# Optimization experiments

Hardware: AMD Instinct MI355X
Metric: run time of the kernel (lower is better)

The kernel has to match this reference:

```python
import jax, jax.numpy as jnp
import numpy as np

NEG = jnp.float32(-1e9)
N_PRE = 12000   # n_train_pre_nms (module default training=True)
N_POST = 2000   # n_train_post_nms
MIN_SIZE = 16.0
NMS_THRESH = 0.7


def _make_anchors(feat_size=64, stride=16):
    scales = np.array([128.0, 256.0, 512.0])
    ratios = np.array([0.5, 1.0, 2.0])
    ws = (scales[:, None] * np.sqrt(1.0 / ratios)[None, :]).reshape(-1)  # [9]
    hs = (scales[:, None] * np.sqrt(ratios)[None, :]).reshape(-1)        # [9]
    ctr = (np.arange(feat_size) + 0.5) * stride
    cy, cx = np.meshgrid(ctr, ctr, indexing='ij')
    cx = cx.reshape(-1, 1); cy = cy.reshape(-1, 1)                       # [4096,1]
    x1 = cx - 0.5 * ws[None, :]; y1 = cy - 0.5 * hs[None, :]
    x2 = cx + 0.5 * ws[None, :]; y2 = cy + 0.5 * hs[None, :]
    return np.stack([x1, y1, x2, y2], axis=-1).reshape(-1, 4).astype(np.float32)  # [36864,4]


def setup_inputs() -> dict:
    key = jax.random.key(0)
    k1, k2 = jax.random.split(key)
    anchors = jnp.asarray(_make_anchors())[None]            # [1, 36864, 4]
    B, N = 8, anchors.shape[1]
    pred_loc = jax.random.normal(k1, (B, N, 4), jnp.float32) * 0.2
    pred_obj = jax.random.normal(k2, (B, N, 2), jnp.float32)
    return {"img_height": 1024, "img_width": 1024,
            "anchor_boxes": anchors, "pred_loc": pred_loc, "pred_obj": pred_obj}


def _decode(anchors, loc, img_w, img_h):
    # anchors [N,4] (x1,y1,x2,y2), loc [N,4] (dx,dy,dw,dh)
    w = anchors[:, 2] - anchors[:, 0]
    h = anchors[:, 3] - anchors[:, 1]
    cx = anchors[:, 0] + 0.5 * w
    cy = anchors[:, 1] + 0.5 * h
    pcx = loc[:, 0] * w + cx
    pcy = loc[:, 1] * h + cy
    pw = jnp.exp(loc[:, 2]) * w
    ph = jnp.exp(loc[:, 3]) * h
    x1 = jnp.clip(pcx - 0.5 * pw, 0.0, img_w)
    y1 = jnp.clip(pcy - 0.5 * ph, 0.0, img_h)
    x2 = jnp.clip(pcx + 0.5 * pw, 0.0, img_w)
    y2 = jnp.clip(pcy + 0.5 * ph, 0.0, img_h)
    return jnp.stack([x1, y1, x2, y2], axis=-1)  # [N,4]


def _iou_one_vs_all(box, boxes):
    # box [4], boxes [M,4]
    ix1 = jnp.maximum(box[0], boxes[:, 0])
    iy1 = jnp.maximum(box[1], boxes[:, 1])
    ix2 = jnp.minimum(box[2], boxes[:, 2])
    iy2 = jnp.minimum(box[3], boxes[:, 3])
    inter = jnp.maximum(ix2 - ix1, 0.0) * jnp.maximum(iy2 - iy1, 0.0)
    a0 = (box[2] - box[0]) * (box[3] - box[1])
    a1 = (boxes[:, 2] - boxes[:, 0]) * (boxes[:, 3] - boxes[:, 1])
    return inter / jnp.maximum(a0 + a1 - inter, 1e-9)


def _greedy_nms(boxes, scores):
    # boxes [M,4], scores [M] (invalid entries already NEG). Selects the first
    # N_POST boxes kept by greedy IoU suppression (exactly torchvision nms +
    # [:n_post] truncation, since greedy NMS emits in descending-score order).
    def step(s, _):
        i = jnp.argmax(s)
        valid = s[i] > NEG * 0.5
        box = boxes[i]
        suppress = _iou_one_vs_all(box, boxes) > NMS_THRESH  # includes self
        s = jnp.where(suppress, NEG, s)
        return s, (box, valid)
    _, (kept, mask) = jax.lax.scan(step, scores, None, length=N_POST)
    return jnp.where(mask[:, None], kept, 0.0), mask  # [N_POST,4], [N_POST]


def reference(img_height, img_width, anchor_boxes, pred_loc, pred_obj):
    img_h = jnp.float32(img_height)
    img_w = jnp.float32(img_width)
    anchors = anchor_boxes[0]                                    # [N,4]
    scores = jax.nn.softmax(pred_obj, axis=2)[:, :, 1]           # [B,N]
    boxes = jax.vmap(lambda l: _decode(anchors, l, img_w, img_h))(pred_loc)  # [B,N,4]
    # min-size filter -> mask scores instead of dynamic filtering
    valid = jnp.all(boxes[..., 2:] - boxes[..., :2] >= MIN_SIZE, axis=-1)    # [B,N]
    scores = jnp.where(valid, scores, NEG)
    # descending sort + pre-NMS truncation == top_k
    top_s, top_i = jax.lax.top_k(scores, N_PRE)                  # [B,N_PRE]
    top_boxes = jnp.take_along_axis(boxes, top_i[..., None], axis=1)         # [B,N_PRE,4]
    kept_boxes, kept_mask = jax.vmap(_greedy_nms)(top_boxes, top_s)
    return kept_boxes, kept_mask  # [B,N_POST,4] padded, [B,N_POST] validity
```

## Files before the change

kernel.cpp:

```cpp
#include <hip/hip_runtime.h>

typedef unsigned long long u64;
typedef unsigned int u32;

#define B_SZ   8
#define N_ANC  36864
#define N_PRE  12000
#define N_POST 2000
#define SEG    2048
#define NSEG   6
#define MAXC   (SEG * NSEG)
#define NW     (SEG / 64)
#define NDW    (MAXC / 64)
#define NBLK   144

__device__ __forceinline__ float area_of(float4 p) {
  return __fmul_rn(__fsub_rn(p.z, p.x), __fsub_rn(p.w, p.y));
}

__device__ __forceinline__ bool iou_gt_a(float4 p, float4 q, float a0, float a1) {
  float ix1 = fmaxf(p.x, q.x), iy1 = fmaxf(p.y, q.y);
  float ix2 = fminf(p.z, q.z), iy2 = fminf(p.w, q.w);
  float iw = fmaxf(__fsub_rn(ix2, ix1), 0.0f);
  float ih = fmaxf(__fsub_rn(iy2, iy1), 0.0f);
  float inter = __fmul_rn(iw, ih);
  float den = fmaxf(__fsub_rn(__fadd_rn(a0, a1), inter), 1e-9f);
  return (inter / den) > 0.7f;
}

__global__ __launch_bounds__(256) void k_decode(
    const int* __restrict__ imh_p, const int* __restrict__ imw_p,
    const float* __restrict__ anchors, const float* __restrict__ loc,
    const float* __restrict__ obj, float4* __restrict__ boxes,
    u64* __restrict__ keys, u32* __restrict__ hist)
{
  __shared__ u32 lh[2048];
  int t = threadIdx.x;
#pragma unroll
  for (int i = 0; i < 8; ++i) lh[t + i * 256] = 0;
  __syncthreads();

  int n = blockIdx.x * 256 + t;
  int b = blockIdx.y;
  float a0 = anchors[n * 4 + 0], a1 = anchors[n * 4 + 1];
  float a2 = anchors[n * 4 + 2], a3 = anchors[n * 4 + 3];
  size_t off = (size_t)b * N_ANC + n;
  float l0 = loc[off * 4 + 0], l1 = loc[off * 4 + 1];
  float l2 = loc[off * 4 + 2], l3 = loc[off * 4 + 3];

  float w  = __fsub_rn(a2, a0);
  float h  = __fsub_rn(a3, a1);
  float cx = __fadd_rn(a0, __fmul_rn(0.5f, w));
  float cy = __fadd_rn(a1, __fmul_rn(0.5f, h));
  float pcx = __fadd_rn(__fmul_rn(l0, w), cx);
  float pcy = __fadd_rn(__fmul_rn(l1, h), cy);
  float pw  = __fmul_rn(expf(l2), w);
  float ph  = __fmul_rn(expf(l3), h);
  float imw = (float)imw_p[0], imh = (float)imh_p[0];
  float hx = __fmul_rn(0.5f, pw), hy = __fmul_rn(0.5f, ph);
  float x1 = fminf(fmaxf(__fsub_rn(pcx, hx), 0.0f), imw);
  float y1 = fminf(fmaxf(__fsub_rn(pcy, hy), 0.0f), imh);
  float x2 = fminf(fmaxf(__fadd_rn(pcx, hx), 0.0f), imw);
  float y2 = fminf(fmaxf(__fadd_rn(pcy, hy), 0.0f), imh);
  boxes[off] = make_float4(x1, y1, x2, y2);

  bool valid = (__fsub_rn(x2, x1) >= 16.0f) && (__fsub_rn(y2, y1) >= 16.0f);

  float o0 = obj[off * 2 + 0], o1 = obj[off * 2 + 1];
  float m  = fmaxf(o0, o1);
  float e0 = expf(__fsub_rn(o0, m));
  float e1 = expf(__fsub_rn(o1, m));
  float s  = e1 / __fadd_rn(e0, e1);
  float sc = valid ? s : -1e9f;

  u32 u  = __float_as_uint(sc);
  u32 fk = (u & 0x80000000u) ? ~u : (u | 0x80000000u);
  u32 sk = ~fk;
  u64 key = ((u64)sk << 32) | (u32)n;
  keys[off] = key;
  atomicAdd(&lh[(u32)(key >> 53)], 1u);
  __syncthreads();
#pragma unroll
  for (int i = 0; i < 8; ++i) {
    u32 v = lh[t + i * 256];
    if (v) atomicAdd(&hist[b * 2048 + t + i * 256], v);
  }
}

__global__ __launch_bounds__(256) void k_pick1(
    const u32* __restrict__ hist, u32* __restrict__ T1, u32* __restrict__ Base1)
{
  int b = blockIdx.x, t = threadIdx.x;
  const u32* h = hist + b * 2048;
  __shared__ u32 part[256], pre[256];
  u32 loc[8], s = 0;
#pragma unroll
  for (int i = 0; i < 8; ++i) { loc[i] = h[t * 8 + i]; s += loc[i]; }
  part[t] = s;
  __syncthreads();
  if (t == 0) { u32 acc = 0; for (int i = 0; i < 256; ++i) { pre[i] = acc; acc += part[i]; } }
  __syncthreads();
  u32 acc = pre[t];
#pragma unroll
  for (int i = 0; i < 8; ++i) {
    u32 na = acc + loc[i];
    if (acc < N_PRE && na >= N_PRE) { T1[b] = (u32)(t * 8 + i); Base1[b] = acc; }
    acc = na;
  }
}

__global__ __launch_bounds__(256) void k_hist2(
    const u64* __restrict__ keys, const u32* __restrict__ T1,
    u32* __restrict__ hist)
{
  int b = blockIdx.y;
  u32 t1 = T1[b];
  __shared__ u32 lh[2048];
  int t = threadIdx.x;
#pragma unroll
  for (int i = 0; i < 8; ++i) lh[t + i * 256] = 0;
  __syncthreads();
#pragma unroll
  for (int k = 0; k < 4; ++k) {
    int i = blockIdx.x * 1024 + k * 256 + t;
    u64 key = keys[(size_t)b * N_ANC + i];
    if ((u32)(key >> 53) == t1) atomicAdd(&lh[(u32)(key >> 42) & 0x7FFu], 1u);
  }
  __syncthreads();
#pragma unroll
  for (int i = 0; i < 8; ++i) {
    u32 v = lh[t + i * 256];
    if (v) atomicAdd(&hist[b * 2048 + t + i * 256], v);
  }
}

__global__ __launch_bounds__(256) void k_pick2(
    const u32* __restrict__ hist, const u32* __restrict__ T1,
    const u32* __restrict__ Base1, u32* __restrict__ T2)
{
  int b = blockIdx.x, t = threadIdx.x;
  const u32* h = hist + b * 2048;
  __shared__ u32 part[256], pre[256];
  u32 loc[8], s = 0;
#pragma unroll
  for (int i = 0; i < 8; ++i) { loc[i] = h[t * 8 + i]; s += loc[i]; }
  part[t] = s;
  __syncthreads();
  if (t == 0) { u32 acc = Base1[b]; for (int i = 0; i < 256; ++i) { pre[i] = acc; acc += part[i]; } }
  __syncthreads();
  u32 acc = pre[t];
#pragma unroll
  for (int i = 0; i < 8; ++i) {
    u32 na = acc + loc[i];
    if (acc < N_PRE && na >= N_PRE) T2[b] = (T1[b] << 11) | (u32)(t * 8 + i);
    acc = na;
  }
}

__global__ __launch_bounds__(256) void k_count(
    const u64* __restrict__ keys, const u32* __restrict__ T2,
    u32* __restrict__ bcnt)
{
  int b = blockIdx.y;
  int i = blockIdx.x * 256 + threadIdx.x;
  u64 key = keys[(size_t)b * N_ANC + i];
  bool pred = (u32)(key >> 42) <= T2[b];
  u64 bal = __ballot(pred);
  __shared__ u32 wc[4];
  int wv = threadIdx.x >> 6, lane = threadIdx.x & 63;
  if (lane == 0) wc[wv] = (u32)__popcll(bal);
  __syncthreads();
  if (threadIdx.x == 0)
    bcnt[b * NBLK + blockIdx.x] = wc[0] + wc[1] + wc[2] + wc[3];
}

__global__ __launch_bounds__(256) void k_scatter(
    const u64* __restrict__ keys, const u32* __restrict__ T2,
    const u32* __restrict__ bcnt, u64* __restrict__ cand)
{
  int b = blockIdx.y, bx = blockIdx.x;
  int t = threadIdx.x;
  __shared__ u32 cnts[NBLK];
  __shared__ u32 wc[4];
  __shared__ u32 sbase;
  if (t < NBLK) cnts[t] = bcnt[b * NBLK + t];
  u64 key = keys[(size_t)b * N_ANC + bx * 256 + t];
  bool pred = (u32)(key >> 42) <= T2[b];
  u64 bal = __ballot(pred);
  int wv = t >> 6, lane = t & 63;
  if (lane == 0) wc[wv] = (u32)__popcll(bal);
  __syncthreads();
  if (t == 0) { u32 a = 0; for (int i = 0; i < bx; ++i) a += cnts[i]; sbase = a; }
  __syncthreads();
  u32 base = sbase;
  for (int w = 0; w < wv; ++w) base += wc[w];
  u32 rank = (u32)__popcll(bal & ((1ull << lane) - 1ull));
  if (pred) {
    u32 pos = base + rank;
    if (pos < MAXC) cand[(size_t)b * MAXC + pos] = key;
  }
}

#define SIDX(x) ((x) + ((x) >> 5))
__global__ __launch_bounds__(1024) void k_sort_tile(u64* __restrict__ a)
{
  int b = blockIdx.y, base = blockIdx.x * 2048;
  u64* p = a + (size_t)b * MAXC + base;
  __shared__ u64 lds[2048 + 64];
  int t = threadIdx.x;
  lds[SIDX(t)] = p[t];
  lds[SIDX(t + 1024)] = p[t + 1024];
  __syncthreads();
  for (int k = 2; k <= 2048; k <<= 1) {
    for (int j = k >> 1; j > 0; j >>= 1) {
      int i = ((t & ~(j - 1)) << 1) | (t & (j - 1));
      int l = i | j;
      bool asc = ((i & k) == 0);
      u64 x = lds[SIDX(i)], y = lds[SIDX(l)];
      if ((x > y) == asc) { lds[SIDX(i)] = y; lds[SIDX(l)] = x; }
      __syncthreads();
    }
  }
  p[t] = lds[SIDX(t)];
  p[t + 1024] = lds[SIDX(t + 1024)];
}

__global__ __launch_bounds__(256) void k_merge_gather(
    const u64* __restrict__ cand, const float4* __restrict__ boxes,
    float4* __restrict__ gbox, u64* __restrict__ deadm)
{
  int b = blockIdx.y;
  int p = blockIdx.x * 256 + threadIdx.x;
  const u64* cb = cand + (size_t)b * MAXC;
  u64 key = cb[p];
  int r = p >> 11;
  int rank = p & 2047;
#pragma unroll
  for (int s = 0; s < NSEG; ++s) {
    if (s == r) continue;
    const u64* run = cb + (s << 11);
    int lo = 0;
#pragma unroll
    for (int step = 2048; step >= 1; step >>= 1) {
      int np = lo + step;
      if (np <= 2048 && run[np - 1] < key) lo = np;
    }
    rank += lo;
  }
  bool valid = ((u32)(key >> 32) < 0x80000000u) && (rank < N_PRE);
  float4 bx = make_float4(0.f, 0.f, 0.f, 0.f);
  if (valid) bx = boxes[(size_t)b * N_ANC + (u32)key];
  gbox[(size_t)b * MAXC + rank] = bx;
  if (!valid) atomicOr(&deadm[b * NDW + (rank >> 6)], 1ull << (rank & 63));
}

__device__ __forceinline__ void segmask_tile_v2(
    int b, int sg, int tile, const float4* __restrict__ gbox,
    u64* __restrict__ smask, u64* __restrict__ smaskT, u64* diag)
{
  int r = tile, rg = 0;
  while (r >= 32 - rg) { r -= 32 - rg; ++rg; }
  int cw = rg + r;
  const float4* gb = gbox + (size_t)b * MAXC + sg * SEG;
  int t = threadIdx.x, wv = t >> 6, lane = t & 63;
  int rbase = rg * 64 + wv * 16;

  float4 rb[16];
#pragma unroll
  for (int i = 0; i < 16; ++i) rb[i] = gb[rbase + i];
  float ra[16];
#pragma unroll
  for (int i = 0; i < 16; ++i) ra[i] = area_of(rb[i]);

  u64* srow = smask + (size_t)(b * NSEG + sg) * SEG * NW + (size_t)rg * 64 * NW;
  float4 cb4 = gb[cw * 64 + lane];
  float ca = area_of(cb4);
  bool isdiag = (cw == rg);
#pragma unroll
  for (int i = 0; i < 16; ++i) {
    int rr = wv * 16 + i;
    bool p = iou_gt_a(rb[i], cb4, ra[i], ca);
    if (isdiag) p = p && (lane > rr);
    u64 m = __ballot(p);
    if (lane == 0) { srow[(size_t)rr * NW + cw] = m; if (isdiag) diag[rr] = m; }
  }
  if (isdiag) {
    __syncthreads();
    if (t < 64) {
      u64 s = 0;
      for (int q = 0; q < 64; ++q) s |= ((diag[q] >> t) & 1ull) << q;
      smaskT[(size_t)(b * NSEG + sg) * SEG + rg * 64 + t] = s;
    }
  }
}

__global__ __launch_bounds__(256) void k_segmask01(
    const float4* __restrict__ gbox, u64* __restrict__ smask,
    u64* __restrict__ smaskT)
{
  __shared__ u64 diag[64];
  int b = blockIdx.y;
  int sg = blockIdx.x / 528, tile = blockIdx.x % 528;
  segmask_tile_v2(b, sg, tile, gbox, smask, smaskT, diag);
}

__device__ __forceinline__ void cross_work(
    int b, int sg, int bx, const float4* __restrict__ gbox,
    const float4* __restrict__ keptb, const int* __restrict__ meta,
    u64* __restrict__ deadm, float4* kb, float* ka)
{
  int kc = bx >> 3, cbk = bx & 7;
  int nkept = meta[b * 8 + 0];
  int kbase = kc * 256;
  if (kbase >= nkept) return;
  int kcnt = min(256, nkept - kbase);
  int t = threadIdx.x;
  if (t < kcnt) {
    float4 k4 = keptb[(size_t)b * SEG + kbase + t];
    kb[t] = k4; ka[t] = area_of(k4);
  }
  __syncthreads();
  int gi = sg * SEG + cbk * 256 + t;
  float4 my = gbox[(size_t)b * MAXC + gi];
  float ma = area_of(my);
  bool sup = false;
  for (int kk = 0; kk < kcnt; ++kk) {
    if (iou_gt_a(kb[kk], my, ka[kk], ma)) { sup = true; break; }
  }
  u64 bm = __ballot(sup);
  if ((t & 63) == 0 && bm) atomicOr(&deadm[b * NDW + (gi >> 6)], bm);
}

__global__ __launch_bounds__(256) void k_cross(
    const float4* __restrict__ gbox, const float4* __restrict__ keptb,
    const int* __restrict__ meta, u64* __restrict__ deadm, int sg)
{
  int b = blockIdx.y;
  if (meta[b * 8 + 1]) return;
  __shared__ float4 kb[256]; __shared__ float ka[256];
  cross_work(b, sg, blockIdx.x, gbox, keptb, meta, deadm, kb, ka);
}

__global__ __launch_bounds__(256) void k_crossmask(
    const float4* __restrict__ gbox, const float4* __restrict__ keptb,
    const int* __restrict__ meta, u64* __restrict__ deadm,
    u64* __restrict__ smask, u64* __restrict__ smaskT, int sg)
{
  int b = blockIdx.y;
  if (meta[b * 8 + 1]) return;
  __shared__ float4 kb[256]; __shared__ float ka[256]; __shared__ u64 diag[64];
  if (blockIdx.x < 64) {
    cross_work(b, sg, blockIdx.x, gbox, keptb, meta, deadm, kb, ka);
  } else {
    segmask_tile_v2(b, sg, blockIdx.x - 64, gbox, smask, smaskT, diag);
  }
}

__global__ __launch_bounds__(1024) void k_walk(
    const float4* __restrict__ gbox, const u64* __restrict__ smask,
    const u64* __restrict__ smaskT, const u64* __restrict__ deadm,
    int* __restrict__ meta, float4* __restrict__ keptb,
    float* __restrict__ out, int sg)
{
  int b = blockIdx.x;
  if (meta[b * 8 + 1]) return;
  int t = threadIdx.x, wv = t >> 6, lane = t & 63;

  __shared__ u64 rowbuf[2][2048];
  __shared__ u64 stbuf[2][64];
  __shared__ float4 bbox[2][64];
  __shared__ u64 sdead[2];
  __shared__ u32 remv[64];
  __shared__ u32 klist[64];
  __shared__ int s_stop, s_nkept, s_kcnt;

  const u64* smb = smask + (size_t)(b * NSEG + sg) * SEG * NW;
  const u64* stb = smaskT + (size_t)(b * NSEG + sg) * SEG;
  const u64* dmb = deadm + b * NDW + sg * NW;
  const float4* gb = gbox + (size_t)b * MAXC + sg * SEG;
  float4* kbuf = keptb + (size_t)b * SEG;
  float4* ob = (float4*)(out + (size_t)b * N_POST * 4);
  float* om = out + (size_t)B_SZ * N_POST * 4 + (size_t)b * N_POST;

  {
    u64 a = smb[t], c = smb[t + 1024];
    u64 st_ = 0; float4 bb_ = make_float4(0.f, 0.f, 0.f, 0.f);
    if (t < 64) { st_ = stb[t]; bb_ = gb[t]; }
    u64 sd_ = (t == 0) ? dmb[0] : 0;
    rowbuf[0][t] = a;
    rowbuf[0][t + 1024] = c;
    if (t < 64) { stbuf[0][t] = st_; bbox[0][t] = bb_; remv[t] = 0; }
    if (t == 0) { sdead[0] = sd_; s_stop = 0; s_nkept = meta[b * 8 + 0]; }
  }
  int p0 = t - 64, p1 = p0 + 960, p2 = p0 + 1920;
  u64 ra = 0, rc = 0, re = 0, rst = 0, rsd = 0;
  float4 rbb = make_float4(0.f, 0.f, 0.f, 0.f);
  if (wv > 0) {
    const u64* src = smb + 2048;
    ra = src[p0];
    rc = src[p1];
    if (p0 < 128) re = src[p2];
    if (p0 < 64) { rst = stb[64 + p0]; rbb = gb[64 + p0]; }
    if (t == 64) rsd = dmb[1];
  }
  __syncthreads();

  for (int g = 0; g < NW; ++g) {
    int cb = g & 1, nb = cb ^ 1;
    if (wv > 0) {
      if (g < NW - 1) {
        rowbuf[nb][p0] = ra;
        rowbuf[nb][p1] = rc;
        if (p0 < 128) rowbuf[nb][p2] = re;
        if (p0 < 64) { stbuf[nb][p0] = rst; bbox[nb][p0] = rbb; }
        if (t == 64) sdead[nb] = rsd;
      }
      if (g < NW - 2) {
        const u64* src = smb + (size_t)(g + 2) * 2048;
        ra = src[p0];
        rc = src[p1];
        if (p0 < 128) re = src[p2];
        if (p0 < 64) { rst = stb[(g + 2) * 64 + p0]; rbb = gb[(g + 2) * 64 + p0]; }
        if (t == 64) rsd = dmb[g + 2];
      }
    } else {
      int l = lane;
      u64 S = stbuf[cb][l];
      u64 remg = ((u64)remv[2 * g + 1] << 32) | remv[2 * g];
      u64 avail = ~(remg | sdead[cb]);
      u64 km = 0;
      while (avail) {
        bool al = (avail >> l) & 1;
        u64 newk = __ballot(al && (S & avail) == 0ull);
        u64 nd   = __ballot(al && (S & newk) != 0ull);
        km |= newk;
        avail &= ~(newk | nd);
      }
      int nk0 = s_nkept;
      int rem = N_POST - nk0;
      int kc = __popcll(km);
      bool stop = (kc >= rem);
      int rank = __popcll(km & ((1ull << l) - 1ull));
      if (((km >> l) & 1) && rank < rem) {
        float4 bx = bbox[cb][l];
        kbuf[nk0 + rank] = bx;
        ob[nk0 + rank] = bx;
        om[nk0 + rank] = 1.0f;
        klist[rank] = (u32)l;
      }
      if (l == 0) {
        int eff = stop ? rem : kc;
        s_kcnt = eff;
        s_nkept = nk0 + eff;
        if (stop) s_stop = 1;
      }
    }
    __syncthreads();
    if (s_stop) break;
    if (g < NW - 1) {
      int kcnt = s_kcnt;
      if (kcnt) {
        u32* rb32 = (u32*)rowbuf[cb];
        for (int i = t; i < kcnt * 64; i += 1024) {
          int kk = i >> 6, w = i & 63;
          if ((w >> 1) > g) {
            u32 v = rb32[klist[kk] * 64 + w];
            if (v) atomicOr(&remv[w], v);
          }
        }
      }
    }
    __syncthreads();
  }
  int nk = s_nkept;
  bool fin = s_stop || (sg == NSEG - 1);
  if (t == 0) { meta[b * 8 + 0] = nk; if (fin) meta[b * 8 + 1] = 1; }
  if (fin) {
    float4 zero = make_float4(0.f, 0.f, 0.f, 0.f);
    for (int i = nk + t; i < N_POST; i += 1024) { ob[i] = zero; om[i] = 0.0f; }
  }
}

extern "C" void kernel_launch(void* const* d_in, const int* in_sizes, int n_in,
                              void* d_out, int out_size, void* d_ws, size_t ws_size,
                              hipStream_t stream)
{
  const int*   imh     = (const int*)d_in[0];
  const int*   imw     = (const int*)d_in[1];
  const float* anchors = (const float*)d_in[2];
  const float* loc     = (const float*)d_in[3];
  const float* obj     = (const float*)d_in[4];
  float* out = (float*)d_out;

  char* ws = (char*)d_ws;
  size_t off = 0;
  float4* boxes = (float4*)(ws + off); off += (size_t)B_SZ * N_ANC * 16;
  u64*    keys  = (u64*)   (ws + off); off += (size_t)B_SZ * N_ANC * 8;
  u64*    cand  = (u64*)   (ws + off); off += (size_t)B_SZ * MAXC * 8;
  float4* gbox  = (float4*)(ws + off); off += (size_t)B_SZ * MAXC * 16;
  float4* keptb = (float4*)(ws + off); off += (size_t)B_SZ * SEG * 16;
  off = (off + 255) & ~(size_t)255;
  char*   zr    = ws + off;
  u32*    hist1 = (u32*)(zr);
  u32*    hist2 = (u32*)(zr + 65536);
  u32*    T1    = (u32*)(zr + 131072);
  u32*    Base1 = (u32*)(zr + 131072 + 32);
  u32*    T2    = (u32*)(zr + 131072 + 64);
  int*    meta  = (int*)(zr + 131072 + 128);
  u64*    deadm = (u64*)(zr + 131072 + 128 + 256);
  u32*    bcnt  = (u32*)(zr + 131072 + 128 + 256 + (size_t)B_SZ * NDW * 8);
  size_t  zr_sz = 131072 + 128 + 256 + (size_t)B_SZ * NDW * 8
                + (size_t)B_SZ * NBLK * 4;
  off += (zr_sz + 255) & ~(size_t)255;
  u64*    smask  = (u64*)(ws + off); off += (size_t)B_SZ * NSEG * SEG * NW * 8;
  u64*    smaskT = (u64*)(ws + off); off += (size_t)B_SZ * NSEG * SEG * 8;

  hipMemsetAsync(zr, 0, zr_sz, stream);
  hipMemsetAsync(cand, 0xFF, (size_t)B_SZ * MAXC * 8, stream);

  k_decode<<<dim3(NBLK, B_SZ), 256, 0, stream>>>(imh, imw, anchors, loc, obj,
                                                 boxes, keys, hist1);
  k_pick1<<<B_SZ, 256, 0, stream>>>(hist1, T1, Base1);
  k_hist2<<<dim3(36, B_SZ), 256, 0, stream>>>(keys, T1, hist2);
  k_pick2<<<B_SZ, 256, 0, stream>>>(hist2, T1, Base1, T2);

  k_count<<<dim3(NBLK, B_SZ), 256, 0, stream>>>(keys, T2, bcnt);
  k_scatter<<<dim3(NBLK, B_SZ), 256, 0, stream>>>(keys, T2, bcnt, cand);

  k_sort_tile<<<dim3(NSEG, B_SZ), 1024, 0, stream>>>(cand);
  k_merge_gather<<<dim3(MAXC / 256, B_SZ), 256, 0, stream>>>(cand, boxes, gbox, deadm);

  k_segmask01<<<dim3(1056, B_SZ), 256, 0, stream>>>(gbox, smask, smaskT);

  k_walk<<<B_SZ, 1024, 0, stream>>>(gbox, smask, smaskT, deadm, meta, keptb, out, 0);
  k_cross<<<dim3(64, B_SZ), 256, 0, stream>>>(gbox, keptb, meta, deadm, 1);
  k_walk<<<B_SZ, 1024, 0, stream>>>(gbox, smask, smaskT, deadm, meta, keptb, out, 1);
  for (int sg = 2; sg < NSEG; ++sg) {
    k_crossmask<<<dim3(592, B_SZ), 256, 0, stream>>>(gbox, keptb, meta, deadm,
                                                     smask, smaskT, sg);
    k_walk<<<B_SZ, 1024, 0, stream>>>(gbox, smask, smaskT, deadm, meta, keptb, out, sg);
  }
}
```

Before: 218.5 us.

## Skip IoU mask work for dead boxes and compute segment 1 mask after cross

The segment mask tile now reads the dead-box bitmask and skips IoU evaluation for rows marked dead, and it writes zeros for whole column words that are entirely dead. The segment 1 mask is no longer built together with segment 0 up front; it is launched after the cross-suppression pass, so boxes already suppressed by segment 0 keeps are skipped, and batches that are already done exit early. This trades one fused launch for an extra kernel launch on the serial path, in exchange for less IoU work.

```diff
diff --git a/kernel.cpp b/kernel.cpp
--- a/kernel.cpp
+++ b/kernel.cpp
@@ -254,35 +254,52 @@
   if (!valid) atomicOr(&deadm[b * NDW + (rank >> 6)], 1ull << (rank & 63));
 }
 
-__device__ __forceinline__ void segmask_tile_v2(
+__device__ __forceinline__ void segmask_tile_v3(
     int b, int sg, int tile, const float4* __restrict__ gbox,
+    const u64* __restrict__ deadm,
     u64* __restrict__ smask, u64* __restrict__ smaskT, u64* diag)
 {
   int r = tile, rg = 0;
   while (r >= 32 - rg) { r -= 32 - rg; ++rg; }
   int cw = rg + r;
   const float4* gb = gbox + (size_t)b * MAXC + sg * SEG;
+  const u64* dmb = deadm + b * NDW + sg * NW;
   int t = threadIdx.x, wv = t >> 6, lane = t & 63;
   int rbase = rg * 64 + wv * 16;
-
-  float4 rb[16];
-#pragma unroll
-  for (int i = 0; i < 16; ++i) rb[i] = gb[rbase + i];
-  float ra[16];
-#pragma unroll
-  for (int i = 0; i < 16; ++i) ra[i] = area_of(rb[i]);
-
+  bool isdiag = (cw == rg);
+  u64 rowdead = dmb[rg];
+  u64 coldead = dmb[cw];
   u64* srow = smask + (size_t)(b * NSEG + sg) * SEG * NW + (size_t)rg * 64 * NW;
-  float4 cb4 = gb[cw * 64 + lane];
-  float ca = area_of(cb4);
-  bool isdiag = (cw == rg);
-#pragma unroll
-  for (int i = 0; i < 16; ++i) {
-    int rr = wv * 16 + i;
-    bool p = iou_gt_a(rb[i], cb4, ra[i], ca);
-    if (isdiag) p = p && (lane > rr);
-    u64 m = __ballot(p);
-    if (lane == 0) { srow[(size_t)rr * NW + cw] = m; if (isdiag) diag[rr] = m; }
+
+  if (coldead == ~0ull) {
+    if (lane == 0) {
+#pragma unroll
+      for (int i = 0; i < 16; ++i) {
+        int rr = wv * 16 + i;
+        srow[(size_t)rr * NW + cw] = 0;
+        if (isdiag) diag[rr] = 0;
+      }
+    }
+  } else {
+    float4 rb[16];
+#pragma unroll
+    for (int i = 0; i < 16; ++i) rb[i] = gb[rbase + i];
+    float ra[16];
+#pragma unroll
+    for (int i = 0; i < 16; ++i) ra[i] = area_of(rb[i]);
+    float4 cb4 = gb[cw * 64 + lane];
+    float ca = area_of(cb4);
+#pragma unroll
+    for (int i = 0; i < 16; ++i) {
+      int rr = wv * 16 + i;
+      u64 m = 0;
+      if (!((rowdead >> rr) & 1)) {
+        bool p = iou_gt_a(rb[i], cb4, ra[i], ca);
+        if (isdiag) p = p && (lane > rr);
+        m = __ballot(p);
+      }
+      if (lane == 0) { srow[(size_t)rr * NW + cw] = m; if (isdiag) diag[rr] = m; }
+    }
   }
   if (isdiag) {
     __syncthreads();
@@ -294,14 +311,15 @@
   }
 }
 
-__global__ __launch_bounds__(256) void k_segmask01(
-    const float4* __restrict__ gbox, u64* __restrict__ smask,
-    u64* __restrict__ smaskT)
+__global__ __launch_bounds__(256) void k_segmask(
+    const float4* __restrict__ gbox, const u64* __restrict__ deadm,
+    const int* __restrict__ meta, u64* __restrict__ smask,
+    u64* __restrict__ smaskT, int sg)
 {
   __shared__ u64 diag[64];
   int b = blockIdx.y;
-  int sg = blockIdx.x / 528, tile = blockIdx.x % 528;
-  segmask_tile_v2(b, sg, tile, gbox, smask, smaskT, diag);
+  if (sg > 0 && meta[b * 8 + 1]) return;
+  segmask_tile_v3(b, sg, blockIdx.x, gbox, deadm, smask, smaskT, diag);
 }
 
 __device__ __forceinline__ void cross_work(
@@ -352,7 +370,7 @@
   if (blockIdx.x < 64) {
     cross_work(b, sg, blockIdx.x, gbox, keptb, meta, deadm, kb, ka);
   } else {
-    segmask_tile_v2(b, sg, blockIdx.x - 64, gbox, smask, smaskT, diag);
+    segmask_tile_v3(b, sg, blockIdx.x - 64, gbox, deadm, smask, smaskT, diag);
   }
 }
 
@@ -530,10 +548,11 @@
   k_sort_tile<<<dim3(NSEG, B_SZ), 1024, 0, stream>>>(cand);
   k_merge_gather<<<dim3(MAXC / 256, B_SZ), 256, 0, stream>>>(cand, boxes, gbox, deadm);
 
-  k_segmask01<<<dim3(1056, B_SZ), 256, 0, stream>>>(gbox, smask, smaskT);
+  k_segmask<<<dim3(528, B_SZ), 256, 0, stream>>>(gbox, deadm, meta, smask, smaskT, 0);
 
   k_walk<<<B_SZ, 1024, 0, stream>>>(gbox, smask, smaskT, deadm, meta, keptb, out, 0);
   k_cross<<<dim3(64, B_SZ), 256, 0, stream>>>(gbox, keptb, meta, deadm, 1);
+  k_segmask<<<dim3(528, B_SZ), 256, 0, stream>>>(gbox, deadm, meta, smask, smaskT, 1);
   k_walk<<<B_SZ, 1024, 0, stream>>>(gbox, smask, smaskT, deadm, meta, keptb, out, 1);
   for (int sg = 2; sg < NSEG; ++sg) {
     k_crossmask<<<dim3(592, B_SZ), 256, 0, stream>>>(gbox, keptb, meta, deadm,
```

After: 226.3 us. 1.04x slower.
